# Kernel tuning notes

Measured on AMD Instinct MI355X. Metric: run time of the kernel, lower is better.

Reference implementation:

```python
import jax, jax.numpy as jnp
import numpy as np

EPS = 1e-5

def _conv3x3(x, w, b):
    # x: (N,C,H,W), w: (O,I,3,3), SAME padding, stride 1
    y = jax.lax.conv_general_dilated(x, w, window_strides=(1, 1), padding='SAME',
                                     dimension_numbers=('NCHW', 'OIHW', 'NCHW'))
    return y + b[None, :, None, None]

def _bn(x, gamma, beta):
    # BatchNorm2d in training mode (batch statistics, biased variance), torch default
    m = jnp.mean(x, axis=(0, 2, 3), keepdims=True)
    v = jnp.var(x, axis=(0, 2, 3), keepdims=True)
    return gamma[None, :, None, None] * (x - m) * jax.lax.rsqrt(v + EPS) + beta[None, :, None, None]

def setup_inputs() -> dict:
    key = jax.random.key(0)
    ks = jax.random.split(key, 12)
    N, T_in, T_out, H, W = 4, 12, 12, 32, 32
    C = 64
    WH = H * W

    def xavier(k, shape, fan_in, fan_out):
        lim = np.sqrt(6.0 / (fan_in + fan_out))
        return jax.random.uniform(k, shape, jnp.float32, -lim, lim)

    x = jax.random.normal(ks[0], (N, T_in, H, W), jnp.float32)
    # ConvBlock: 5 conv(3x3)+BN+ReLU layers; first conv is T_in->64, rest 64->64
    conv0_w = xavier(ks[1], (C, T_in, 3, 3), T_in * 9, C * 9)
    conv_w = xavier(ks[2], (4, C, C, 3, 3), C * 9, C * 9)
    conv_b = jnp.zeros((5, C), jnp.float32)
    bn_gamma = jnp.ones((5, C), jnp.float32)
    bn_beta = jnp.zeros((5, C), jnp.float32)
    reg_w = xavier(ks[3], (T_out, C, 3, 3), C * 9, T_out * 9)
    reg_b = jnp.zeros((T_out,), jnp.float32)
    # attention weight (timesteps=12, WH, WH), xavier_uniform
    att_w = xavier(ks[4], (12, WH, WH), WH, WH)
    return {'x': x, 'conv0_w': conv0_w, 'conv_w': conv_w, 'conv_b': conv_b,
            'bn_gamma': bn_gamma, 'bn_beta': bn_beta,
            'reg_w': reg_w, 'reg_b': reg_b, 'att_w': att_w}

def reference(x, conv0_w, conv_w, conv_b, bn_gamma, bn_beta, reg_w, reg_b, att_w):
    h = x
    for i in range(5):
        w = conv0_w if i == 0 else conv_w[i - 1]
        h = jax.nn.relu(_bn(_conv3x3(h, w, conv_b[i]), bn_gamma[i], bn_beta[i]))
    h = _conv3x3(h, reg_w, reg_b)  # (N, T, H, W)
    N, T, H, W = h.shape
    WH = H * W
    xf = h.reshape(N, T, WH)
    # hadamard attention: xp[n,t,i,j] = xf[n,t,j]; scores = weight * xp
    scores = att_w[None, :, :, :] * xf[:, :, None, :]  # (N,T,WH,WH)
    att = jax.nn.softmax(scores, axis=3)
    out = jnp.einsum('ntij,ntj->nti', att, xf).reshape(N, T, H, W)
    return out, att
```

## Files before the change

kernel.cpp:

```cpp
#include <hip/hip_runtime.h>

#define EPS_BN 1e-5f

typedef float f32x4 __attribute__((ext_vector_type(4)));

#define PROWS 34
#define PCOLS 36
#define PS (PROWS * PCOLS)

__global__ __launch_bounds__(256) void pad_copy_kern(
    const float* __restrict__ x, float* __restrict__ bufX)
{
    const int plane = blockIdx.x;
    const int tid = threadIdx.x;
    const int r  = tid >> 3;
    const int c4 = (tid & 7) << 2;
    float4 v = *(const float4*)(x + (plane << 10) + (r << 5) + c4);
    float* o = bufX + plane * PS + (r + 1) * PCOLS + (c4 + 1);
    o[0] = v.x; o[1] = v.y; o[2] = v.z; o[3] = v.w;
}

template<int CIN, int COUT, bool BN_IN, bool STATS, bool PAD_OUT>
__global__ __launch_bounds__(256) void conv3x3_v2(
    const float* __restrict__ in,
    const float* __restrict__ wgt,
    const float* __restrict__ bias,
    const float* __restrict__ in_stats,
    const float* __restrict__ gamma,
    const float* __restrict__ beta,
    float* __restrict__ out,
    float* __restrict__ out_stats)
{
    __shared__ float s_sc[64];
    __shared__ float s_sh[64];
    __shared__ float s_corr[8];

    const int tid = threadIdx.x;
    const int n   = blockIdx.x / COUT;
    const int co  = blockIdx.x - n * COUT;

    if (BN_IN) {
        if (tid < CIN) {
            float s    = in_stats[tid];
            float ss   = in_stats[64 + tid];
            float mean = s * (1.0f / 4096.0f);
            float var  = fmaxf(ss * (1.0f / 4096.0f) - mean * mean, 0.0f);
            float g    = gamma[tid] * rsqrtf(var + EPS_BN);
            float sc   = g;
            float sh   = beta[tid] - mean * g;
            s_sc[tid] = sc;
            s_sh[tid] = sh;
            float rl = fmaxf(sh, 0.0f);
            const float* wp = wgt + (co * CIN + tid) * 9;
            float w0=wp[0], w1=wp[1], w2=wp[2], w3=wp[3],
                  w5=wp[5], w6=wp[6], w7=wp[7], w8=wp[8];
            float pT  = rl * (w0 + w1 + w2);
            float pB  = rl * (w6 + w7 + w8);
            float pL  = rl * (w0 + w3 + w6);
            float pR  = rl * (w2 + w5 + w8);
            float pTL = rl * w0, pTR = rl * w2, pBL = rl * w6, pBR = rl * w8;
            #pragma unroll
            for (int off = 32; off; off >>= 1) {
                pT  += __shfl_down(pT,  off); pB  += __shfl_down(pB,  off);
                pL  += __shfl_down(pL,  off); pR  += __shfl_down(pR,  off);
                pTL += __shfl_down(pTL, off); pTR += __shfl_down(pTR, off);
                pBL += __shfl_down(pBL, off); pBR += __shfl_down(pBR, off);
            }
            if (tid == 0) {
                s_corr[0]=pT; s_corr[1]=pB; s_corr[2]=pL; s_corr[3]=pR;
                s_corr[4]=pTL; s_corr[5]=pTR; s_corr[6]=pBL; s_corr[7]=pBR;
            }
        }
        __syncthreads();
    }

    const int r  = tid >> 3;
    const int c4 = (tid & 7) << 2;
    const float* ip = in + n * CIN * PS + r * PCOLS + c4;

    float acc0 = 0.f, acc1 = 0.f, acc2 = 0.f, acc3 = 0.f;

    #pragma unroll 2
    for (int ci = 0; ci < CIN; ++ci) {
        const float* p  = ip + ci * PS;
        const float* wp = wgt + (co * CIN + ci) * 9;
        float sc = 0.f, sh = 0.f;
        if (BN_IN) { sc = s_sc[ci]; sh = s_sh[ci]; }
        #pragma unroll
        for (int dr = 0; dr < 3; ++dr) {
            float4 a = *(const float4*)(p + dr * PCOLS);
            float2 b = *(const float2*)(p + dr * PCOLS + 4);
            float h0, h1, h2, h3, h4, h5;
            if (BN_IN) {
                h0 = fmaxf(fmaf(sc, a.x, sh), 0.f);
                h1 = fmaxf(fmaf(sc, a.y, sh), 0.f);
                h2 = fmaxf(fmaf(sc, a.z, sh), 0.f);
                h3 = fmaxf(fmaf(sc, a.w, sh), 0.f);
                h4 = fmaxf(fmaf(sc, b.x, sh), 0.f);
                h5 = fmaxf(fmaf(sc, b.y, sh), 0.f);
            } else {
                h0 = a.x; h1 = a.y; h2 = a.z; h3 = a.w; h4 = b.x; h5 = b.y;
            }
            float wa = wp[dr * 3 + 0], wb = wp[dr * 3 + 1], wc = wp[dr * 3 + 2];
            acc0 = fmaf(wa, h0, fmaf(wb, h1, fmaf(wc, h2, acc0)));
            acc1 = fmaf(wa, h1, fmaf(wb, h2, fmaf(wc, h3, acc1)));
            acc2 = fmaf(wa, h2, fmaf(wb, h3, fmaf(wc, h4, acc2)));
            acc3 = fmaf(wa, h3, fmaf(wb, h4, fmaf(wc, h5, acc3)));
        }
    }

    float bv = bias[co];
    float u0 = acc0 + bv, u1 = acc1 + bv, u2 = acc2 + bv, u3 = acc3 + bv;

    if (BN_IN) {
        float corr = (r == 0 ? s_corr[0] : 0.f) + (r == 31 ? s_corr[1] : 0.f);
        u0 -= corr; u1 -= corr; u2 -= corr; u3 -= corr;
        if (c4 == 0) {
            u0 -= s_corr[2];
            if (r == 0)  u0 += s_corr[4];
            if (r == 31) u0 += s_corr[6];
        }
        if (c4 == 28) {
            u3 -= s_corr[3];
            if (r == 0)  u3 += s_corr[5];
            if (r == 31) u3 += s_corr[7];
        }
    }

    if (PAD_OUT) {
        float* op = out + (n * COUT + co) * PS + (r + 1) * PCOLS + (c4 + 1);
        op[0] = u0; op[1] = u1; op[2] = u2; op[3] = u3;
    } else {
        float4 res; res.x = u0; res.y = u1; res.z = u2; res.w = u3;
        *(float4*)(out + ((n * COUT + co) << 10) + (r << 5) + c4) = res;
    }

    if (STATS) {
        float s  = u0 + u1 + u2 + u3;
        float ss = u0*u0 + u1*u1 + u2*u2 + u3*u3;
        #pragma unroll
        for (int off = 32; off; off >>= 1) {
            s  += __shfl_down(s,  off);
            ss += __shfl_down(ss, off);
        }
        if ((tid & 63) == 0) {
            atomicAdd(&out_stats[co],      s);
            atomicAdd(&out_stats[64 + co], ss);
        }
    }
}

__global__ __launch_bounds__(256) void attention_v2(
    const float* __restrict__ xf,
    const float* __restrict__ att_w,
    float* __restrict__ out,
    float* __restrict__ att)
{
    __shared__ __align__(16) float s_xf[4096];
    __shared__ float red[4][8];
    const int tid = threadIdx.x;
    const int t   = blockIdx.x >> 10;
    const int i   = blockIdx.x & 1023;
    const int w   = tid >> 6;

    const float4* xf4 = (const float4*)xf;
    float4* s4 = (float4*)s_xf;
    #pragma unroll
    for (int q = 0; q < 4; ++q) {
        int e  = (q << 8) + tid;
        int nn = e >> 8;
        int j4 = e & 255;
        s4[e] = xf4[((nn * 12 + t) << 8) + j4];
    }
    float4 wv = ((const float4*)att_w)[(((t << 10) + i) << 8) + tid];
    __syncthreads();

    float ev[4][4], ps[4], pd[4];
    #pragma unroll
    for (int nn = 0; nn < 4; ++nn) {
        float4 xv = ((const float4*)(s_xf + (nn << 10)))[tid];
        float e0 = __expf(wv.x * xv.x);
        float e1 = __expf(wv.y * xv.y);
        float e2 = __expf(wv.z * xv.z);
        float e3 = __expf(wv.w * xv.w);
        ps[nn] = (e0 + e1) + (e2 + e3);
        pd[nn] = fmaf(e0, xv.x, fmaf(e1, xv.y, fmaf(e2, xv.z, e3 * xv.w)));
        ev[nn][0] = e0; ev[nn][1] = e1; ev[nn][2] = e2; ev[nn][3] = e3;
    }
    #pragma unroll
    for (int off = 32; off; off >>= 1) {
        #pragma unroll
        for (int nn = 0; nn < 4; ++nn) {
            ps[nn] += __shfl_down(ps[nn], off);
            pd[nn] += __shfl_down(pd[nn], off);
        }
    }
    if ((tid & 63) == 0) {
        #pragma unroll
        for (int nn = 0; nn < 4; ++nn) {
            red[w][nn]     = ps[nn];
            red[w][4 + nn] = pd[nn];
        }
    }
    __syncthreads();

    #pragma unroll
    for (int nn = 0; nn < 4; ++nn) {
        float sum = (red[0][nn] + red[1][nn]) + (red[2][nn] + red[3][nn]);
        float dot = (red[0][4+nn] + red[1][4+nn]) + (red[2][4+nn] + red[3][4+nn]);
        float inv = 1.0f / sum;
        f32x4 av;
        av.x = ev[nn][0] * inv; av.y = ev[nn][1] * inv;
        av.z = ev[nn][2] * inv; av.w = ev[nn][3] * inv;
        f32x4* dst = (f32x4*)att + ((((nn * 12 + t) << 10) + i) << 8) + tid;
        __builtin_nontemporal_store(av, dst);
        if (tid == 0) out[((nn * 12 + t) << 10) + i] = dot * inv;
    }
}

extern "C" void kernel_launch(void* const* d_in, const int* in_sizes, int n_in,
                              void* d_out, int out_size, void* d_ws, size_t ws_size,
                              hipStream_t stream)
{
    const float* x      = (const float*)d_in[0];
    const float* conv0w = (const float*)d_in[1];
    const float* convw  = (const float*)d_in[2];
    const float* convb  = (const float*)d_in[3];
    const float* gammas = (const float*)d_in[4];
    const float* betas  = (const float*)d_in[5];
    const float* regw   = (const float*)d_in[6];
    const float* regb   = (const float*)d_in[7];
    const float* attw   = (const float*)d_in[8];

    float* out = (float*)d_out;
    float* att = out + 4 * 12 * 1024;

    float* ws    = (float*)d_ws;
    float* stats = ws;
    float* bufX  = stats + 640;
    float* bufA  = bufX + 48 * PS;
    float* bufB  = bufA + 256 * PS;
    float* xf    = bufB + 256 * PS;

    (void)hipMemsetAsync(stats, 0,
                         (640 + 48 * PS + 2 * 256 * PS) * sizeof(float),
                         stream);

    pad_copy_kern<<<48, 256, 0, stream>>>(x, bufX);

    conv3x3_v2<12, 64, false, true, true><<<256, 256, 0, stream>>>(
        bufX, conv0w, convb, nullptr, nullptr, nullptr, bufA, stats);
    conv3x3_v2<64, 64, true, true, true><<<256, 256, 0, stream>>>(
        bufA, convw + 0 * 36864, convb + 64, stats, gammas, betas,
        bufB, stats + 128);
    conv3x3_v2<64, 64, true, true, true><<<256, 256, 0, stream>>>(
        bufB, convw + 1 * 36864, convb + 128, stats + 128, gammas + 64,
        betas + 64, bufA, stats + 256);
    conv3x3_v2<64, 64, true, true, true><<<256, 256, 0, stream>>>(
        bufA, convw + 2 * 36864, convb + 192, stats + 256, gammas + 128,
        betas + 128, bufB, stats + 384);
    conv3x3_v2<64, 64, true, true, true><<<256, 256, 0, stream>>>(
        bufB, convw + 3 * 36864, convb + 256, stats + 384, gammas + 192,
        betas + 192, bufA, stats + 512);
    conv3x3_v2<64, 12, true, false, false><<<48, 256, 0, stream>>>(
        bufA, regw, regb, stats + 512, gammas + 256, betas + 256, xf, nullptr);

    attention_v2<<<12288, 256, 0, stream>>>(xf, attw, out, att);
}
```

Baseline: 399.7 us.

## Split conv input channels across blocks with combine and separate BN-ReLU kernels

Each conv layer is split into four input-channel chunks computed by separate blocks that write partial sums, followed by a combine kernel that adds bias and gathers BN stats, then an in-place BN+ReLU pass. The aim is to give the GPU four times as many blocks per conv (1024 instead of 256) and to drop the per-element BN transform inside the inner loop. The partial buffer reuses the att output region as scratch. In exchange it adds extra kernel launches and global round trips for the partial sums and the BN pass.

```diff
diff --git a/kernel.cpp b/kernel.cpp
--- a/kernel.cpp
+++ b/kernel.cpp
@@ -20,124 +20,85 @@
     o[0] = v.x; o[1] = v.y; o[2] = v.z; o[3] = v.w;
 }
 
-template<int CIN, int COUT, bool BN_IN, bool STATS, bool PAD_OUT>
-__global__ __launch_bounds__(256) void conv3x3_v2(
+template<int CI_CHUNK, int CIN, int COUT>
+__global__ __launch_bounds__(256) void conv3x3_part(
     const float* __restrict__ in,
     const float* __restrict__ wgt,
+    float* __restrict__ part)
+{
+    const int tid = threadIdx.x;
+    const int b   = blockIdx.x;
+    const int PL4   = 4 * COUT;
+    const int chunk = b / PL4;
+    const int rem   = b - chunk * PL4;
+    const int n     = rem / COUT;
+    const int co    = rem - n * COUT;
+    const int ci0   = chunk * CI_CHUNK;
+
+    const int r  = tid >> 3;
+    const int c4 = (tid & 7) << 2;
+    const float* ip  = in + (n * CIN + ci0) * PS + r * PCOLS + c4;
+    const float* wp0 = wgt + (co * CIN + ci0) * 9;
+
+    float acc0 = 0.f, acc1 = 0.f, acc2 = 0.f, acc3 = 0.f;
+
+    #pragma unroll 4
+    for (int ci = 0; ci < CI_CHUNK; ++ci) {
+        const float* p  = ip + ci * PS;
+        const float* wp = wp0 + ci * 9;
+        #pragma unroll
+        for (int dr = 0; dr < 3; ++dr) {
+            float4 a  = *(const float4*)(p + dr * PCOLS);
+            float2 bb = *(const float2*)(p + dr * PCOLS + 4);
+            float wa = wp[dr * 3 + 0], wb = wp[dr * 3 + 1], wc = wp[dr * 3 + 2];
+            acc0 = fmaf(wa, a.x, fmaf(wb, a.y, fmaf(wc, a.z, acc0)));
+            acc1 = fmaf(wa, a.y, fmaf(wb, a.z, fmaf(wc, a.w, acc1)));
+            acc2 = fmaf(wa, a.z, fmaf(wb, a.w, fmaf(wc, bb.x, acc2)));
+            acc3 = fmaf(wa, a.w, fmaf(wb, bb.x, fmaf(wc, bb.y, acc3)));
+        }
+    }
+
+    f32x4 res; res.x = acc0; res.y = acc1; res.z = acc2; res.w = acc3;
+    *((f32x4*)part + (b << 8) + tid) = res;
+}
+
+template<int COUT, bool STATS, bool PAD_OUT>
+__global__ __launch_bounds__(256) void combine_kern(
+    const float* __restrict__ part,
     const float* __restrict__ bias,
-    const float* __restrict__ in_stats,
-    const float* __restrict__ gamma,
-    const float* __restrict__ beta,
     float* __restrict__ out,
     float* __restrict__ out_stats)
 {
-    __shared__ float s_sc[64];
-    __shared__ float s_sh[64];
-    __shared__ float s_corr[8];
-
-    const int tid = threadIdx.x;
-    const int n   = blockIdx.x / COUT;
-    const int co  = blockIdx.x - n * COUT;
-
-    if (BN_IN) {
-        if (tid < CIN) {
-            float s    = in_stats[tid];
-            float ss   = in_stats[64 + tid];
-            float mean = s * (1.0f / 4096.0f);
-            float var  = fmaxf(ss * (1.0f / 4096.0f) - mean * mean, 0.0f);
-            float g    = gamma[tid] * rsqrtf(var + EPS_BN);
-            float sc   = g;
-            float sh   = beta[tid] - mean * g;
-            s_sc[tid] = sc;
-            s_sh[tid] = sh;
-            float rl = fmaxf(sh, 0.0f);
-            const float* wp = wgt + (co * CIN + tid) * 9;
-            float w0=wp[0], w1=wp[1], w2=wp[2], w3=wp[3],
-                  w5=wp[5], w6=wp[6], w7=wp[7], w8=wp[8];
-            float pT  = rl * (w0 + w1 + w2);
-            float pB  = rl * (w6 + w7 + w8);
-            float pL  = rl * (w0 + w3 + w6);
-            float pR  = rl * (w2 + w5 + w8);
-            float pTL = rl * w0, pTR = rl * w2, pBL = rl * w6, pBR = rl * w8;
-            #pragma unroll
-            for (int off = 32; off; off >>= 1) {
-                pT  += __shfl_down(pT,  off); pB  += __shfl_down(pB,  off);
-                pL  += __shfl_down(pL,  off); pR  += __shfl_down(pR,  off);
-                pTL += __shfl_down(pTL, off); pTR += __shfl_down(pTR, off);
-                pBL += __shfl_down(pBL, off); pBR += __shfl_down(pBR, off);
-            }
-            if (tid == 0) {
-                s_corr[0]=pT; s_corr[1]=pB; s_corr[2]=pL; s_corr[3]=pR;
-                s_corr[4]=pTL; s_corr[5]=pTR; s_corr[6]=pBL; s_corr[7]=pBR;
-            }
-        }
-        __syncthreads();
-    }
-
-    const int r  = tid >> 3;
-    const int c4 = (tid & 7) << 2;
-    const float* ip = in + n * CIN * PS + r * PCOLS + c4;
-
-    float acc0 = 0.f, acc1 = 0.f, acc2 = 0.f, acc3 = 0.f;
-
-    #pragma unroll 2
-    for (int ci = 0; ci < CIN; ++ci) {
-        const float* p  = ip + ci * PS;
-        const float* wp = wgt + (co * CIN + ci) * 9;
-        float sc = 0.f, sh = 0.f;
-        if (BN_IN) { sc = s_sc[ci]; sh = s_sh[ci]; }
-        #pragma unroll
-        for (int dr = 0; dr < 3; ++dr) {
-            float4 a = *(const float4*)(p + dr * PCOLS);
-            float2 b = *(const float2*)(p + dr * PCOLS + 4);
-            float h0, h1, h2, h3, h4, h5;
-            if (BN_IN) {
-                h0 = fmaxf(fmaf(sc, a.x, sh), 0.f);
-                h1 = fmaxf(fmaf(sc, a.y, sh), 0.f);
-                h2 = fmaxf(fmaf(sc, a.z, sh), 0.f);
-                h3 = fmaxf(fmaf(sc, a.w, sh), 0.f);
-                h4 = fmaxf(fmaf(sc, b.x, sh), 0.f);
-                h5 = fmaxf(fmaf(sc, b.y, sh), 0.f);
-            } else {
-                h0 = a.x; h1 = a.y; h2 = a.z; h3 = a.w; h4 = b.x; h5 = b.y;
-            }
-            float wa = wp[dr * 3 + 0], wb = wp[dr * 3 + 1], wc = wp[dr * 3 + 2];
-            acc0 = fmaf(wa, h0, fmaf(wb, h1, fmaf(wc, h2, acc0)));
-            acc1 = fmaf(wa, h1, fmaf(wb, h2, fmaf(wc, h3, acc1)));
-            acc2 = fmaf(wa, h2, fmaf(wb, h3, fmaf(wc, h4, acc2)));
-            acc3 = fmaf(wa, h3, fmaf(wb, h4, fmaf(wc, h5, acc3)));
-        }
-    }
-
-    float bv = bias[co];
-    float u0 = acc0 + bv, u1 = acc1 + bv, u2 = acc2 + bv, u3 = acc3 + bv;
-
-    if (BN_IN) {
-        float corr = (r == 0 ? s_corr[0] : 0.f) + (r == 31 ? s_corr[1] : 0.f);
-        u0 -= corr; u1 -= corr; u2 -= corr; u3 -= corr;
-        if (c4 == 0) {
-            u0 -= s_corr[2];
-            if (r == 0)  u0 += s_corr[4];
-            if (r == 31) u0 += s_corr[6];
-        }
-        if (c4 == 28) {
-            u3 -= s_corr[3];
-            if (r == 0)  u3 += s_corr[5];
-            if (r == 31) u3 += s_corr[7];
-        }
-    }
+    const int tid = threadIdx.x;
+    const int p   = blockIdx.x;
+    const int NP  = 4 * COUT;
+    const int co  = p - (p / COUT) * COUT;
+
+    const float4* pp = (const float4*)part + (p << 8) + tid;
+    const int cs = NP << 8;
+    float4 a = pp[0];
+    float4 b = pp[cs];
+    float4 c = pp[2 * cs];
+    float4 d = pp[3 * cs];
+    const float bv = bias[co];
+    float u0 = ((a.x + b.x) + (c.x + d.x)) + bv;
+    float u1 = ((a.y + b.y) + (c.y + d.y)) + bv;
+    float u2 = ((a.z + b.z) + (c.z + d.z)) + bv;
+    float u3 = ((a.w + b.w) + (c.w + d.w)) + bv;
 
     if (PAD_OUT) {
-        float* op = out + (n * COUT + co) * PS + (r + 1) * PCOLS + (c4 + 1);
-        op[0] = u0; op[1] = u1; op[2] = u2; op[3] = u3;
+        const int r  = tid >> 3;
+        const int c4 = (tid & 7) << 2;
+        float* o = out + p * PS + (r + 1) * PCOLS + (c4 + 1);
+        o[0] = u0; o[1] = u1; o[2] = u2; o[3] = u3;
     } else {
-        float4 res; res.x = u0; res.y = u1; res.z = u2; res.w = u3;
-        *(float4*)(out + ((n * COUT + co) << 10) + (r << 5) + c4) = res;
+        f32x4 res; res.x = u0; res.y = u1; res.z = u2; res.w = u3;
+        *((f32x4*)out + (p << 8) + tid) = res;
     }
 
     if (STATS) {
         float s  = u0 + u1 + u2 + u3;
-        float ss = u0*u0 + u1*u1 + u2*u2 + u3*u3;
+        float ss = u0 * u0 + u1 * u1 + u2 * u2 + u3 * u3;
         #pragma unroll
         for (int off = 32; off; off >>= 1) {
             s  += __shfl_down(s,  off);
@@ -148,6 +109,32 @@
             atomicAdd(&out_stats[64 + co], ss);
         }
     }
+}
+
+__global__ __launch_bounds__(256) void bnrelu_kern(
+    float* __restrict__ buf,
+    const float* __restrict__ stats,
+    const float* __restrict__ gamma,
+    const float* __restrict__ beta)
+{
+    const int tid = threadIdx.x;
+    const int p   = blockIdx.x;
+    const int ch  = p & 63;
+
+    const float s    = stats[ch];
+    const float ss   = stats[64 + ch];
+    const float mean = s * (1.0f / 4096.0f);
+    const float var  = fmaxf(ss * (1.0f / 4096.0f) - mean * mean, 0.0f);
+    const float g    = gamma[ch] * rsqrtf(var + EPS_BN);
+    const float sh   = beta[ch] - mean * g;
+
+    const int r  = tid >> 3;
+    const int c4 = (tid & 7) << 2;
+    float* o = buf + p * PS + (r + 1) * PCOLS + (c4 + 1);
+    o[0] = fmaxf(fmaf(g, o[0], sh), 0.f);
+    o[1] = fmaxf(fmaf(g, o[1], sh), 0.f);
+    o[2] = fmaxf(fmaf(g, o[2], sh), 0.f);
+    o[3] = fmaxf(fmaf(g, o[3], sh), 0.f);
 }
 
 __global__ __launch_bounds__(256) void attention_v2(
@@ -241,6 +228,7 @@
     float* bufA  = bufX + 48 * PS;
     float* bufB  = bufA + 256 * PS;
     float* xf    = bufB + 256 * PS;
+    float* part  = att;
 
     (void)hipMemsetAsync(stats, 0,
                          (640 + 48 * PS + 2 * 256 * PS) * sizeof(float),
@@ -248,22 +236,28 @@
 
     pad_copy_kern<<<48, 256, 0, stream>>>(x, bufX);
 
-    conv3x3_v2<12, 64, false, true, true><<<256, 256, 0, stream>>>(
-        bufX, conv0w, convb, nullptr, nullptr, nullptr, bufA, stats);
-    conv3x3_v2<64, 64, true, true, true><<<256, 256, 0, stream>>>(
-        bufA, convw + 0 * 36864, convb + 64, stats, gammas, betas,
-        bufB, stats + 128);
-    conv3x3_v2<64, 64, true, true, true><<<256, 256, 0, stream>>>(
-        bufB, convw + 1 * 36864, convb + 128, stats + 128, gammas + 64,
-        betas + 64, bufA, stats + 256);
-    conv3x3_v2<64, 64, true, true, true><<<256, 256, 0, stream>>>(
-        bufA, convw + 2 * 36864, convb + 192, stats + 256, gammas + 128,
-        betas + 128, bufB, stats + 384);
-    conv3x3_v2<64, 64, true, true, true><<<256, 256, 0, stream>>>(
-        bufB, convw + 3 * 36864, convb + 256, stats + 384, gammas + 192,
-        betas + 192, bufA, stats + 512);
-    conv3x3_v2<64, 12, true, false, false><<<48, 256, 0, stream>>>(
-        bufA, regw, regb, stats + 512, gammas + 256, betas + 256, xf, nullptr);
+    conv3x3_part<3, 12, 64><<<1024, 256, 0, stream>>>(bufX, conv0w, part);
+    combine_kern<64, true, true><<<256, 256, 0, stream>>>(part, convb, bufA, stats);
+    bnrelu_kern<<<256, 256, 0, stream>>>(bufA, stats, gammas, betas);
+
+    conv3x3_part<16, 64, 64><<<1024, 256, 0, stream>>>(bufA, convw + 0 * 36864, part);
+    combine_kern<64, true, true><<<256, 256, 0, stream>>>(part, convb + 64, bufB, stats + 128);
+    bnrelu_kern<<<256, 256, 0, stream>>>(bufB, stats + 128, gammas + 64, betas + 64);
+
+    conv3x3_part<16, 64, 64><<<1024, 256, 0, stream>>>(bufB, convw + 1 * 36864, part);
+    combine_kern<64, true, true><<<256, 256, 0, stream>>>(part, convb + 128, bufA, stats + 256);
+    bnrelu_kern<<<256, 256, 0, stream>>>(bufA, stats + 256, gammas + 128, betas + 128);
+
+    conv3x3_part<16, 64, 64><<<1024, 256, 0, stream>>>(bufA, convw + 2 * 36864, part);
+    combine_kern<64, true, true><<<256, 256, 0, stream>>>(part, convb + 192, bufB, stats + 384);
+    bnrelu_kern<<<256, 256, 0, stream>>>(bufB, stats + 384, gammas + 192, betas + 192);
+
+    conv3x3_part<16, 64, 64><<<1024, 256, 0, stream>>>(bufB, convw + 3 * 36864, part);
+    combine_kern<64, true, true><<<256, 256, 0, stream>>>(part, convb + 256, bufA, stats + 512);
+    bnrelu_kern<<<256, 256, 0, stream>>>(bufA, stats + 512, gammas + 256, betas + 256);
+
+    conv3x3_part<16, 64, 12><<<192, 256, 0, stream>>>(bufA, regw, part);
+    combine_kern<12, false, false><<<48, 256, 0, stream>>>(part, regb, xf, nullptr);
 
     attention_v2<<<12288, 256, 0, stream>>>(xf, attw, out, att);
 }
```

Result: slower. 409.0 us (+2.3%).
